# Kernel optimization log

Hardware: AMD Instinct MI355X
Metric: run time of the kernel (lower is better)

Reference implementation:

```python
import jax, jax.numpy as jnp
import numpy as np

B, P, C, H, W = 2, 4, 3, 256, 256
BGH, BGW = 2764, 3856
NOISE_MU, NOISE_SIGMA, NOISE_POISSON, BG_RATIO = 5.0, 1.0, 2.0, 0.1


def setup_inputs() -> dict:
    key = jax.random.key(0)
    k_x, k_bg = jax.random.split(key, 2)
    x = jax.random.uniform(k_x, (B, P, C, H, W), dtype=jnp.float32)
    t = jnp.array([0.05, 0.1, 0.15, 0.2], dtype=jnp.float32)          # Time_init (len p)
    ratio = jnp.ones((P,), dtype=jnp.float32)
    life = jnp.array([100.0, 200.0, 300.0], dtype=jnp.float32)         # flo_life (len c)
    intensity_ratio = jnp.array([1.0, 0.8, 0.6], dtype=jnp.float32)    # flo_intensity_ratio
    bg_file = jax.random.uniform(k_bg, (P, BGH, BGW), dtype=jnp.float32)
    return {"x": x, "t": t, "ratio": ratio, "life": life,
            "intensity_ratio": intensity_ratio, "bg_file": bg_file}


def reference(x, t, ratio, life, intensity_ratio, bg_file):
    b, p, c, h, w = x.shape
    key = jax.random.key(42)
    k_life, k_sig, k_norm, k_p1, k_p2, k_bg1, k_bg2, k_bgn, k_idx = jax.random.split(key, 9)

    # Time = relu((t*ratio)*1000), per-p scalar broadcast over (b,c,h,w)
    Time = jnp.maximum((t * ratio) * 1000.0, 0.0)                      # (p,)

    # tao_i: 9-point linspace around each lifetime, concatenated -> (T,) with T = 9*c
    tao = (life[:, None] + jnp.linspace(-40.0, 40.0, 9)).reshape(-1)   # (9c,)

    Life = life[None, None, :, None, None]                             # (1,1,c,1,1)
    Life_rand = Life + (jax.random.uniform(k_life, (b, p, c, h, w)) - 0.5) * 2.0 * 6.0
    sigma = 6.0
    sigma_rand = sigma + (jax.random.uniform(k_sig, (b, p, c, h, w)) - 0.5) * 2.0 * sigma * 0.05

    tao6 = tao[:, None, None, None, None, None]                        # (T,1,1,1,1,1)
    # Gaussian weights over the tao axis (matches torch's 3.14 constant)
    w_i = jnp.exp(-(tao6 - Life_rand) ** 2 / (2.0 * sigma_rand ** 2)) / (
        jnp.sqrt(jnp.float32(2.0 * 3.14)) * sigma_rand)                # (T,b,p,c,h,w)
    w_i = w_i / w_i.sum(axis=0)

    # tao_gt: sum over c, mean over p, permute -> (b,T,h,w), detached
    tao_gt = jax.lax.stop_gradient(jnp.transpose(w_i.sum(axis=3).mean(axis=2), (1, 0, 2, 3)))

    # decay_metrics = sum_T w_i * exp(-Time/tao); exp term only depends on (T,p)
    et = jnp.exp(-Time[None, :] / tao[:, None])                        # (T,p)
    decay = jnp.einsum('tp,tbpchw->bpchw', et, w_i)                    # (b,p,c,h,w)

    x2 = (x * decay * intensity_ratio[None, None, :, None, None]).sum(axis=2)  # (b,p,h,w)

    # noise(): Normal + Poisson(x/max) + Poisson(const) + x (samples detached in torch)
    xm = x2 / (x2.max() + 0.0001)
    n_int = xm * NOISE_MU + NOISE_SIGMA * jax.random.normal(k_norm, x2.shape)
    p_int = jax.random.poisson(k_p1, jnp.maximum(xm, 0.0)).astype(x2.dtype)
    pois = jax.random.poisson(k_p2, jnp.full(x2.shape, NOISE_POISSON)).astype(x2.dtype)
    x3 = n_int + p_int + pois + x2

    # bg(): scaled background file + noise, random 256x256 row offset
    bg1 = jax.random.uniform(k_bg1, (b, p, 1, 1)) * 0.5 + 0.5
    bg2 = jax.random.uniform(k_bg2, (b, p, 1, 1)) * 0.5 + 0.5
    bgn = jax.random.normal(k_bgn, (b, p, BGH, BGW))
    GRR = (bg_file[None] * bg1 + bgn * bg2) * BG_RATIO                 # (b,p,BGH,BGW)
    idx = jax.random.randint(k_idx, (), 0, 9)
    patch = jax.lax.dynamic_slice(GRR, (0, 0, idx, 0), (b, p, 256, 256))
    x4 = jnp.clip(x3 + patch, 0.0, 255.0) / 255.0

    return (x4, tao_gt, t * ratio, ratio)
```

## Files before the change

### kernel.cpp

```cpp
#include <hip/hip_runtime.h>
#include <cstdint>
#include <cstddef>

#define BB 2
#define PP 4
#define CC 3
#define HWSZ 65536
#define BGH 2764
#define BGW 3856
#define NTAO 27
#define X4_SIZE (BB*PP*HWSZ)
#define TAO_OFF X4_SIZE
#define TAO_SIZE (BB*NTAO*HWSZ)
#define OUT2_OFF (TAO_OFF + TAO_SIZE)
#define NPK 24
#define NBLK_A 2048

__host__ __device__ inline uint32_t rotl32(uint32_t x, int r) {
#ifdef __HIP_DEVICE_COMPILE__
  return __builtin_amdgcn_alignbit(x, x, 32 - r);
#else
  return (x << r) | (x >> (32 - r));
#endif
}

__host__ __device__ inline void tf2x32(uint32_t k0, uint32_t k1,
                                       uint32_t x0, uint32_t x1,
                                       uint32_t& o0, uint32_t& o1) {
  uint32_t ks2 = k0 ^ k1 ^ 0x1BD11BDAu;
  x0 += k0; x1 += k1;
#define TF_RND(r) { x0 += x1; x1 = rotl32(x1, r); x1 ^= x0; }
  TF_RND(13) TF_RND(15) TF_RND(26) TF_RND(6)
  x0 += k1;  x1 += ks2 + 1u;
  TF_RND(17) TF_RND(29) TF_RND(16) TF_RND(24)
  x0 += ks2; x1 += k0 + 2u;
  TF_RND(13) TF_RND(15) TF_RND(26) TF_RND(6)
  x0 += k0;  x1 += k1 + 3u;
  TF_RND(17) TF_RND(29) TF_RND(16) TF_RND(24)
  x0 += k1;  x1 += ks2 + 4u;
  TF_RND(13) TF_RND(15) TF_RND(26) TF_RND(6)
  x0 += ks2; x1 += k0 + 5u;
#undef TF_RND
  o0 = x0; o1 = x1;
}

__host__ __device__ inline uint32_t bits32(uint32_t k0, uint32_t k1, uint32_t e) {
  uint32_t o0, o1;
  tf2x32(k0, k1, 0u, e, o0, o1);
  return o0 ^ o1;
}

static void jax_split(uint32_t k0, uint32_t k1, int n, uint32_t (*keys)[2]) {
  for (int i = 0; i < n; ++i)
    tf2x32(k0, k1, 0u, (uint32_t)i, keys[i][0], keys[i][1]);
}

__host__ __device__ inline float u01(uint32_t bits) {
  uint32_t fb = (bits >> 9) | 0x3F800000u;
  return __builtin_bit_cast(float, fb) - 1.0f;
}

__device__ inline float erfinv_f(float x) {
  float w = -log1pf(-x * x);
  float p;
  if (w < 5.0f) {
    w = w - 2.5f;
    p = 2.81022636e-08f;
    p = fmaf(p, w, 3.43273939e-07f);
    p = fmaf(p, w, -3.5233877e-06f);
    p = fmaf(p, w, -4.39150654e-06f);
    p = fmaf(p, w, 0.00021858087f);
    p = fmaf(p, w, -0.00125372503f);
    p = fmaf(p, w, -0.00417768164f);
    p = fmaf(p, w, 0.246640727f);
    p = fmaf(p, w, 1.50140941f);
  } else {
    w = sqrtf(w) - 3.0f;
    p = -0.000200214257f;
    p = fmaf(p, w, 0.000100950558f);
    p = fmaf(p, w, 0.00134934322f);
    p = fmaf(p, w, -0.00367342844f);
    p = fmaf(p, w, 0.00573950773f);
    p = fmaf(p, w, -0.0076224613f);
    p = fmaf(p, w, 0.00943887047f);
    p = fmaf(p, w, 1.00167406f);
    p = fmaf(p, w, 2.83297682f);
  }
  return p * x;
}

__device__ inline float normal_e(uint32_t k0, uint32_t k1, uint32_t e) {
  float f = u01(bits32(k0, k1, e));
  const float LO = -0.99999994f;
  float u = fmaxf(LO, fmaf(f, 2.0f, LO));
  return 1.41421356237f * erfinv_f(u);
}

struct PCParams {
  uint32_t kn0, kn1;
  uint32_t kb0, kb1;
  uint32_t s1[NPK * 2];
  uint32_t s2[NPK * 2];
  float bg1[8], bg2[8];
  int idx;
};

__device__ inline float decay_pc(uint32_t kl0, uint32_t kl1, uint32_t ks0,
                                 uint32_t ks1, uint32_t e,
                                 const float (*et)[4], int p, float* tg9) {
  float ul = u01(bits32(kl0, kl1, e));
  float us = u01(bits32(ks0, ks1, e));
  float d0 = -40.0f - (ul - 0.5f) * 12.0f;
  float sr = fmaf(us - 0.5f, 0.6f, 6.0f);
  float inv = __builtin_amdgcn_rcpf(2.0f * sr * sr);
  float q[9];
  float A  = __expf(-20.0f * inv * d0);
  float Bm = __expf(-100.0f * inv);
  float B2 = Bm * Bm;
  q[0] = __expf(-(d0 * d0) * inv);
  float m = A * Bm;
  float s = q[0];
#pragma unroll
  for (int j = 1; j < 9; ++j) {
    q[j] = q[j - 1] * m;
    m *= B2;
    s += q[j];
  }
  float rs = __builtin_amdgcn_rcpf(s);
  float dec = 0.0f;
#pragma unroll
  for (int j = 0; j < 9; ++j) {
    float wn = q[j] * rs;
    tg9[j] += wn;
    dec = fmaf(et[j][p], wn, dec);
  }
  return dec;
}

__global__ __launch_bounds__(256) void kA(
    const float* __restrict__ x, const float* __restrict__ t,
    const float* __restrict__ ratio, const float* __restrict__ life,
    const float* __restrict__ inten, float* __restrict__ out,
    float* __restrict__ bmax,
    uint32_t kl0, uint32_t kl1, uint32_t ks0, uint32_t ks1) {
  __shared__ float tao_s[NTAO];
  __shared__ float et_s[NTAO][4];
  __shared__ float inten_s[3];
  __shared__ float tg_lds[4][9][64];
  __shared__ float bmax_s[4];
  const int tid = threadIdx.x;
  if (tid < NTAO * 4) {
    int j = tid >> 2, p = tid & 3;
    float tao = life[j / 9] + (-40.0f + 10.0f * (float)(j % 9));
    float Tp = fmaxf(t[p] * ratio[p] * 1000.0f, 0.0f);
    et_s[j][p] = expf((-Tp) / tao);
    if (p == 0) tao_s[j] = tao;
  }
  if (tid < 3) inten_s[tid] = inten[tid];
  __syncthreads();

  const int blk = blockIdx.x;
  const int b = blk >> 10;
  const int hwg = blk & 1023;
  const int p = tid >> 6;
  const int lane = tid & 63;
  const int hw = hwg * 64 + lane;

  float acc = 0.0f;

  for (int c = 0; c < 3; ++c) {
    float tg9[9];
#pragma unroll
    for (int j = 0; j < 9; ++j) tg9[j] = 0.0f;

    const uint32_t e = (uint32_t)((((b * 4 + p) * 3 + c) << 16) + hw);
    float dec = decay_pc(kl0, kl1, ks0, ks1, e,
                         (const float(*)[4])&et_s[c * 9], p, tg9);
    acc = fmaf(x[e] * dec, inten_s[c], acc);

#pragma unroll
    for (int j = 0; j < 9; ++j) tg_lds[p][j][lane] = tg9[j];
    __syncthreads();
    for (int jj = p; jj < 9; jj += 4) {
      float s = ((tg_lds[0][jj][lane] + tg_lds[1][jj][lane]) +
                 (tg_lds[2][jj][lane] + tg_lds[3][jj][lane]));
      out[TAO_OFF + ((b * NTAO + c * 9 + jj) << 16) + hw] = s * 0.25f;
    }
    __syncthreads();
  }

  out[((b * 4 + p) << 16) + hw] = acc;

  float m = acc;
#pragma unroll
  for (int off = 32; off; off >>= 1) m = fmaxf(m, __shfl_xor(m, off));
  if (lane == 0) bmax_s[p] = m;
  __syncthreads();
  if (tid == 0)
    bmax[blk] = fmaxf(fmaxf(bmax_s[0], bmax_s[1]),
                      fmaxf(bmax_s[2], bmax_s[3]));
}

__global__ __launch_bounds__(1024) void kMax(const float* __restrict__ bmax,
                                             float* __restrict__ maxslot) {
  __shared__ float red[16];
  const int tid = threadIdx.x;
  float m = fmaxf(bmax[tid], bmax[tid + 1024]);
#pragma unroll
  for (int off = 32; off; off >>= 1) m = fmaxf(m, __shfl_xor(m, off));
  if ((tid & 63) == 0) red[tid >> 6] = m;
  __syncthreads();
  if (tid == 0) {
    float mm = red[0];
#pragma unroll
    for (int i = 1; i < 16; ++i) mm = fmaxf(mm, red[i]);
    maxslot[0] = mm;
  }
}

__global__ __launch_bounds__(256) void kC(
    const float* __restrict__ bgf, const float* __restrict__ t,
    const float* __restrict__ ratio, float* __restrict__ out,
    const float* __restrict__ maxslot, PCParams pc) {
  const int e = blockIdx.x * 256 + threadIdx.x;
  if (blockIdx.x == 0 && threadIdx.x < 8) {
    int i = threadIdx.x;
    out[OUT2_OFF + i] = (i < 4) ? t[i] * ratio[i] : ratio[i - 4];
  }
  const int bp = e >> 16;
  const int rcc = e & 0xFFFF;
  const int r = rcc >> 8;
  const int cc = rcc & 255;

  const int row = pc.idx + r;
  const int p = bp & 3;
  float bg = bgf[(p * BGH + row) * BGW + cc];
  const uint32_t ebg = (uint32_t)((bp * BGH + row) * BGW + cc);
  float nb = normal_e(pc.kb0, pc.kb1, ebg);
  float patch = (bg * pc.bg1[bp] + nb * pc.bg2[bp]) * 0.1f;

  float n = normal_e(pc.kn0, pc.kn1, (uint32_t)e);

  const float x2 = out[e];
  const float mx = maxslot[0];
  const float xm = x2 / (mx + 0.0001f);
  float n_int = xm * 5.0f + 1.0f * n;

  float lam1 = fmaxf(xm, 0.0f);
  const bool z1 = !(lam1 > 0.0f);
  float lp1 = 0.0f, lp2 = 0.0f;
  int k1 = 0, k2 = 0;
#pragma clang loop unroll(disable)
  for (int i = 0; i < NPK; ++i) {
    bool c1 = (!z1) && (lp1 > -lam1);
    bool c2 = (lp2 > -2.0f);
    if (!(c1 || c2)) break;
    if (c1) { k1++; lp1 += __logf(u01(bits32(pc.s1[2*i], pc.s1[2*i+1], (uint32_t)e))); }
    if (c2) { k2++; lp2 += __logf(u01(bits32(pc.s2[2*i], pc.s2[2*i+1], (uint32_t)e))); }
  }
  float pi = z1 ? 0.0f : (float)(k1 - 1);
  float po = (float)(k2 - 1);

  float x3 = ((n_int + pi) + po) + x2;
  float v = x3 + patch;
  v = fminf(fmaxf(v, 0.0f), 255.0f);
  out[e] = v / 255.0f;
}

extern "C" void kernel_launch(void* const* d_in, const int* in_sizes, int n_in,
                              void* d_out, int out_size, void* d_ws, size_t ws_size,
                              hipStream_t stream) {
  const float* x     = (const float*)d_in[0];
  const float* t     = (const float*)d_in[1];
  const float* ratio = (const float*)d_in[2];
  const float* life  = (const float*)d_in[3];
  const float* inten = (const float*)d_in[4];
  const float* bgf   = (const float*)d_in[5];
  float* out = (float*)d_out;
  float* bmax = (float*)d_ws;
  float* maxslot = bmax + NBLK_A;

  uint32_t sk[9][2];
  jax_split(0u, 42u, 9, sk);

  PCParams pc;
  pc.kn0 = sk[2][0]; pc.kn1 = sk[2][1];
  pc.kb0 = sk[7][0]; pc.kb1 = sk[7][1];

  {
    uint32_t r0 = sk[3][0], r1 = sk[3][1];
    for (int i = 0; i < NPK; ++i) {
      uint32_t two[2][2];
      jax_split(r0, r1, 2, two);
      pc.s1[2*i] = two[1][0]; pc.s1[2*i+1] = two[1][1];
      r0 = two[0][0]; r1 = two[0][1];
    }
    r0 = sk[4][0]; r1 = sk[4][1];
    for (int i = 0; i < NPK; ++i) {
      uint32_t two[2][2];
      jax_split(r0, r1, 2, two);
      pc.s2[2*i] = two[1][0]; pc.s2[2*i+1] = two[1][1];
      r0 = two[0][0]; r1 = two[0][1];
    }
  }

  for (uint32_t i = 0; i < 8; ++i) {
    pc.bg1[i] = u01(bits32(sk[5][0], sk[5][1], i)) * 0.5f + 0.5f;
    pc.bg2[i] = u01(bits32(sk[6][0], sk[6][1], i)) * 0.5f + 0.5f;
  }

  {
    uint32_t hi = bits32(sk[8][0], sk[8][1], 0u);
    uint32_t lo = bits32(sk[8][0], sk[8][1], 1u);
    const uint32_t span = 9u;
    uint32_t mult = (65536u % span);
    mult = (mult * mult) % span;
    uint32_t off = ((hi % span) * mult + (lo % span)) % span;
    pc.idx = (int)off;
  }

  kA<<<NBLK_A, 256, 0, stream>>>(x, t, ratio, life, inten, out, bmax,
                                 sk[0][0], sk[0][1], sk[1][0], sk[1][1]);
  kMax<<<1, 1024, 0, stream>>>(bmax, maxslot);
  kC<<<X4_SIZE / 256, 256, 0, stream>>>(bgf, t, ratio, out, maxslot, pc);
}
```

Baseline: 40.52 us.

## Fold max reduction into kC, split noise work across thread pairs, batch tao_gt stores

Removes the separate single-block max kernel: every kC block now re-reduces the 2048 per-block maxima itself. kC launches two threads per output element, one doing the normal noise plus the const-rate Poisson loop and the other doing the background noise plus the data-dependent Poisson loop. Partial results are exchanged with a lane shuffle, so the serial Poisson loops of the two draws run in parallel rather than back to back. In kA, the tao_gt staging buffer now holds all three channels so only one barrier is needed, and the unused tao_s array is removed. The cost is redundant max reads in every kC block, twice as many kC threads, and more LDS per kA block.

```diff
diff --git a/kernel.cpp b/kernel.cpp
--- a/kernel.cpp
+++ b/kernel.cpp
@@ -143,10 +143,9 @@
     const float* __restrict__ inten, float* __restrict__ out,
     float* __restrict__ bmax,
     uint32_t kl0, uint32_t kl1, uint32_t ks0, uint32_t ks1) {
-  __shared__ float tao_s[NTAO];
   __shared__ float et_s[NTAO][4];
   __shared__ float inten_s[3];
-  __shared__ float tg_lds[4][9][64];
+  __shared__ float tg_lds[4][NTAO][64];
   __shared__ float bmax_s[4];
   const int tid = threadIdx.x;
   if (tid < NTAO * 4) {
@@ -154,7 +153,6 @@
     float tao = life[j / 9] + (-40.0f + 10.0f * (float)(j % 9));
     float Tp = fmaxf(t[p] * ratio[p] * 1000.0f, 0.0f);
     et_s[j][p] = expf((-Tp) / tao);
-    if (p == 0) tao_s[j] = tao;
   }
   if (tid < 3) inten_s[tid] = inten[tid];
   __syncthreads();
@@ -168,6 +166,7 @@
 
   float acc = 0.0f;
 
+#pragma unroll
   for (int c = 0; c < 3; ++c) {
     float tg9[9];
 #pragma unroll
@@ -179,14 +178,16 @@
     acc = fmaf(x[e] * dec, inten_s[c], acc);
 
 #pragma unroll
-    for (int j = 0; j < 9; ++j) tg_lds[p][j][lane] = tg9[j];
-    __syncthreads();
-    for (int jj = p; jj < 9; jj += 4) {
-      float s = ((tg_lds[0][jj][lane] + tg_lds[1][jj][lane]) +
-                 (tg_lds[2][jj][lane] + tg_lds[3][jj][lane]));
-      out[TAO_OFF + ((b * NTAO + c * 9 + jj) << 16) + hw] = s * 0.25f;
-    }
-    __syncthreads();
+    for (int j = 0; j < 9; ++j) tg_lds[p][c * 9 + j][lane] = tg9[j];
+  }
+  __syncthreads();
+
+#pragma unroll
+  for (int it = tid; it < NTAO * 64; it += 256) {
+    int row = it >> 6, ln = it & 63;
+    float s = ((tg_lds[0][row][ln] + tg_lds[1][row][ln]) +
+               (tg_lds[2][row][ln] + tg_lds[3][row][ln]));
+    out[TAO_OFF + ((b * NTAO + row) << 16) + hwg * 64 + ln] = s * 0.25f;
   }
 
   out[((b * 4 + p) << 16) + hw] = acc;
@@ -201,70 +202,82 @@
                       fmaxf(bmax_s[2], bmax_s[3]));
 }
 
-__global__ __launch_bounds__(1024) void kMax(const float* __restrict__ bmax,
-                                             float* __restrict__ maxslot) {
-  __shared__ float red[16];
-  const int tid = threadIdx.x;
-  float m = fmaxf(bmax[tid], bmax[tid + 1024]);
-#pragma unroll
-  for (int off = 32; off; off >>= 1) m = fmaxf(m, __shfl_xor(m, off));
-  if ((tid & 63) == 0) red[tid >> 6] = m;
-  __syncthreads();
-  if (tid == 0) {
-    float mm = red[0];
-#pragma unroll
-    for (int i = 1; i < 16; ++i) mm = fmaxf(mm, red[i]);
-    maxslot[0] = mm;
-  }
-}
-
 __global__ __launch_bounds__(256) void kC(
     const float* __restrict__ bgf, const float* __restrict__ t,
     const float* __restrict__ ratio, float* __restrict__ out,
-    const float* __restrict__ maxslot, PCParams pc) {
-  const int e = blockIdx.x * 256 + threadIdx.x;
-  if (blockIdx.x == 0 && threadIdx.x < 8) {
-    int i = threadIdx.x;
-    out[OUT2_OFF + i] = (i < 4) ? t[i] * ratio[i] : ratio[i - 4];
-  }
+    const float* __restrict__ bmax, PCParams pc) {
+  __shared__ float red_s[4];
+  __shared__ float mx_s;
+  const int tid = threadIdx.x;
+
+  float m = 0.0f;
+#pragma unroll
+  for (int k = 0; k < 8; ++k) m = fmaxf(m, bmax[tid + 256 * k]);
+#pragma unroll
+  for (int off = 32; off; off >>= 1) m = fmaxf(m, __shfl_xor(m, off));
+  if ((tid & 63) == 0) red_s[tid >> 6] = m;
+  __syncthreads();
+  if (tid == 0)
+    mx_s = fmaxf(fmaxf(red_s[0], red_s[1]), fmaxf(red_s[2], red_s[3]));
+  __syncthreads();
+  const float mx = mx_s;
+
+  if (blockIdx.x == 0 && tid < 8)
+    out[OUT2_OFF + tid] = (tid < 4) ? t[tid] * ratio[tid] : ratio[tid - 4];
+
+  const int t2 = blockIdx.x * 256 + tid;
+  const int e = t2 >> 1;
+  const int parity = t2 & 1;
+
   const int bp = e >> 16;
   const int rcc = e & 0xFFFF;
   const int r = rcc >> 8;
   const int cc = rcc & 255;
 
+  const float x2 = out[e];
+  const float xm = x2 * __builtin_amdgcn_rcpf(mx + 0.0001f);
+
   const int row = pc.idx + r;
-  const int p = bp & 3;
-  float bg = bgf[(p * BGH + row) * BGW + cc];
+  const int pp = bp & 3;
   const uint32_t ebg = (uint32_t)((bp * BGH + row) * BGW + cc);
-  float nb = normal_e(pc.kb0, pc.kb1, ebg);
-  float patch = (bg * pc.bg1[bp] + nb * pc.bg2[bp]) * 0.1f;
-
-  float n = normal_e(pc.kn0, pc.kn1, (uint32_t)e);
-
-  const float x2 = out[e];
-  const float mx = maxslot[0];
-  const float xm = x2 / (mx + 0.0001f);
-  float n_int = xm * 5.0f + 1.0f * n;
-
-  float lam1 = fmaxf(xm, 0.0f);
-  const bool z1 = !(lam1 > 0.0f);
-  float lp1 = 0.0f, lp2 = 0.0f;
-  int k1 = 0, k2 = 0;
+  uint32_t nk0 = parity ? pc.kb0 : pc.kn0;
+  uint32_t nk1 = parity ? pc.kb1 : pc.kn1;
+  uint32_t ne  = parity ? ebg : (uint32_t)e;
+  float nval = normal_e(nk0, nk1, ne);
+
+  float patch = 0.0f;
+  if (parity) {
+    float bg = bgf[(pp * BGH + row) * BGW + cc];
+    patch = (bg * pc.bg1[bp] + nval * pc.bg2[bp]) * 0.1f;
+  }
+
+  float lam = parity ? fmaxf(xm, 0.0f) : 2.0f;
+  const bool zz = !(lam > 0.0f);
+  const float neg = -lam;
+  float lp = 0.0f;
+  int k = 0;
 #pragma clang loop unroll(disable)
   for (int i = 0; i < NPK; ++i) {
-    bool c1 = (!z1) && (lp1 > -lam1);
-    bool c2 = (lp2 > -2.0f);
-    if (!(c1 || c2)) break;
-    if (c1) { k1++; lp1 += __logf(u01(bits32(pc.s1[2*i], pc.s1[2*i+1], (uint32_t)e))); }
-    if (c2) { k2++; lp2 += __logf(u01(bits32(pc.s2[2*i], pc.s2[2*i+1], (uint32_t)e))); }
-  }
-  float pi = z1 ? 0.0f : (float)(k1 - 1);
-  float po = (float)(k2 - 1);
-
-  float x3 = ((n_int + pi) + po) + x2;
-  float v = x3 + patch;
-  v = fminf(fmaxf(v, 0.0f), 255.0f);
-  out[e] = v / 255.0f;
+    bool c = (!zz) && (lp > neg);
+    if (!__any(c)) break;
+    if (c) {
+      k++;
+      uint32_t key0 = parity ? pc.s1[2 * i]     : pc.s2[2 * i];
+      uint32_t key1 = parity ? pc.s1[2 * i + 1] : pc.s2[2 * i + 1];
+      lp += __logf(u01(bits32(key0, key1, (uint32_t)e)));
+    }
+  }
+  float pk = zz ? 0.0f : (float)(k - 1);
+
+  float pi_o    = __shfl_xor(pk, 1);
+  float patch_o = __shfl_xor(patch, 1);
+
+  if (!parity) {
+    float n_int = fmaf(xm, 5.0f, nval);
+    float v = (((n_int + pi_o) + pk) + x2) + patch_o;
+    v = fminf(fmaxf(v, 0.0f), 255.0f);
+    out[e] = v * (1.0f / 255.0f);
+  }
 }
 
 extern "C" void kernel_launch(void* const* d_in, const int* in_sizes, int n_in,
@@ -278,7 +291,6 @@
   const float* bgf   = (const float*)d_in[5];
   float* out = (float*)d_out;
   float* bmax = (float*)d_ws;
-  float* maxslot = bmax + NBLK_A;
 
   uint32_t sk[9][2];
   jax_split(0u, 42u, 9, sk);
@@ -321,6 +333,5 @@
 
   kA<<<NBLK_A, 256, 0, stream>>>(x, t, ratio, life, inten, out, bmax,
                                  sk[0][0], sk[0][1], sk[1][0], sk[1][1]);
-  kMax<<<1, 1024, 0, stream>>>(bmax, maxslot);
-  kC<<<X4_SIZE / 256, 256, 0, stream>>>(bgf, t, ratio, out, maxslot, pc);
-}
+  kC<<<(2 * X4_SIZE) / 256, 256, 0, stream>>>(bgf, t, ratio, out, bmax, pc);
+}
```

After: 43.27 us. 6.8% more time.

## Fuse max reduction into kC, batch Poisson sampling, use fast intrinsics

Applied to the files above, without the earlier changes.

Removes the separate single-block max kernel: each kC block re-reduces the 2048 per-block maxima itself, saving one launch and its serialization gap at the cost of redundant reads. The Poisson sampling loop is rewritten to process four uniforms per step with wave-uniform (__any) exit checks, reducing branch divergence and loop overhead but computing some extra random numbers. erfinv, the normalization and the final scaling switch to fast log, sqrt, rcp and multiply intrinsics, which may change precision slightly.

```diff
diff --git a/kernel.cpp b/kernel.cpp
--- a/kernel.cpp
+++ b/kernel.cpp
@@ -14,6 +14,7 @@
 #define TAO_SIZE (BB*NTAO*HWSZ)
 #define OUT2_OFF (TAO_OFF + TAO_SIZE)
 #define NPK 24
+#define NPB 4
 #define NBLK_A 2048
 
 __host__ __device__ inline uint32_t rotl32(uint32_t x, int r) {
@@ -61,7 +62,7 @@
 }
 
 __device__ inline float erfinv_f(float x) {
-  float w = -log1pf(-x * x);
+  float w = -__logf(fmaf(-x, x, 1.0f));
   float p;
   if (w < 5.0f) {
     w = w - 2.5f;
@@ -75,7 +76,7 @@
     p = fmaf(p, w, 0.246640727f);
     p = fmaf(p, w, 1.50140941f);
   } else {
-    w = sqrtf(w) - 3.0f;
+    w = __builtin_amdgcn_sqrtf(w) - 3.0f;
     p = -0.000200214257f;
     p = fmaf(p, w, 0.000100950558f);
     p = fmaf(p, w, 0.00134934322f);
@@ -104,6 +105,23 @@
   float bg1[8], bg2[8];
   int idx;
 };
+
+__device__ inline void pk_batch(const uint32_t* __restrict__ sk, int b,
+                                uint32_t e, float neg, float& lp, int& k) {
+  float l0 = __logf(u01(bits32(sk[(b*NPB+0)*2], sk[(b*NPB+0)*2+1], e)));
+  float l1 = __logf(u01(bits32(sk[(b*NPB+1)*2], sk[(b*NPB+1)*2+1], e)));
+  float l2 = __logf(u01(bits32(sk[(b*NPB+2)*2], sk[(b*NPB+2)*2+1], e)));
+  float l3 = __logf(u01(bits32(sk[(b*NPB+3)*2], sk[(b*NPB+3)*2+1], e)));
+  int cnt = (lp > neg) ? 1 : 0;
+  float p0 = lp + l0;
+  cnt += (p0 > neg) ? 1 : 0;
+  float p1 = p0 + l1;
+  cnt += (p1 > neg) ? 1 : 0;
+  float p2 = p1 + l2;
+  cnt += (p2 > neg) ? 1 : 0;
+  lp = p2 + l3;
+  k += cnt;
+}
 
 __device__ inline float decay_pc(uint32_t kl0, uint32_t kl1, uint32_t ks0,
                                  uint32_t ks1, uint32_t e,
@@ -143,7 +161,6 @@
     const float* __restrict__ inten, float* __restrict__ out,
     float* __restrict__ bmax,
     uint32_t kl0, uint32_t kl1, uint32_t ks0, uint32_t ks1) {
-  __shared__ float tao_s[NTAO];
   __shared__ float et_s[NTAO][4];
   __shared__ float inten_s[3];
   __shared__ float tg_lds[4][9][64];
@@ -154,7 +171,6 @@
     float tao = life[j / 9] + (-40.0f + 10.0f * (float)(j % 9));
     float Tp = fmaxf(t[p] * ratio[p] * 1000.0f, 0.0f);
     et_s[j][p] = expf((-Tp) / tao);
-    if (p == 0) tao_s[j] = tao;
   }
   if (tid < 3) inten_s[tid] = inten[tid];
   __syncthreads();
@@ -201,32 +217,30 @@
                       fmaxf(bmax_s[2], bmax_s[3]));
 }
 
-__global__ __launch_bounds__(1024) void kMax(const float* __restrict__ bmax,
-                                             float* __restrict__ maxslot) {
-  __shared__ float red[16];
-  const int tid = threadIdx.x;
-  float m = fmaxf(bmax[tid], bmax[tid + 1024]);
-#pragma unroll
-  for (int off = 32; off; off >>= 1) m = fmaxf(m, __shfl_xor(m, off));
-  if ((tid & 63) == 0) red[tid >> 6] = m;
-  __syncthreads();
-  if (tid == 0) {
-    float mm = red[0];
-#pragma unroll
-    for (int i = 1; i < 16; ++i) mm = fmaxf(mm, red[i]);
-    maxslot[0] = mm;
-  }
-}
-
 __global__ __launch_bounds__(256) void kC(
     const float* __restrict__ bgf, const float* __restrict__ t,
     const float* __restrict__ ratio, float* __restrict__ out,
-    const float* __restrict__ maxslot, PCParams pc) {
-  const int e = blockIdx.x * 256 + threadIdx.x;
-  if (blockIdx.x == 0 && threadIdx.x < 8) {
-    int i = threadIdx.x;
-    out[OUT2_OFF + i] = (i < 4) ? t[i] * ratio[i] : ratio[i - 4];
-  }
+    const float* __restrict__ bmax, PCParams pc) {
+  __shared__ float red_s[4];
+  __shared__ float mx_s;
+  const int tid = threadIdx.x;
+
+  float m = 0.0f;
+#pragma unroll
+  for (int k = 0; k < 8; ++k) m = fmaxf(m, bmax[tid + 256 * k]);
+#pragma unroll
+  for (int off = 32; off; off >>= 1) m = fmaxf(m, __shfl_xor(m, off));
+  if ((tid & 63) == 0) red_s[tid >> 6] = m;
+  __syncthreads();
+  if (tid == 0)
+    mx_s = fmaxf(fmaxf(red_s[0], red_s[1]), fmaxf(red_s[2], red_s[3]));
+  __syncthreads();
+  const float mx = mx_s;
+
+  if (blockIdx.x == 0 && tid < 8)
+    out[OUT2_OFF + tid] = (tid < 4) ? t[tid] * ratio[tid] : ratio[tid - 4];
+
+  const int e = blockIdx.x * 256 + tid;
   const int bp = e >> 16;
   const int rcc = e & 0xFFFF;
   const int r = rcc >> 8;
@@ -234,29 +248,29 @@
 
   const int row = pc.idx + r;
   const int p = bp & 3;
-  float bg = bgf[(p * BGH + row) * BGW + cc];
+  const float bg = bgf[(p * BGH + row) * BGW + cc];
+  const float x2 = out[e];
+
   const uint32_t ebg = (uint32_t)((bp * BGH + row) * BGW + cc);
   float nb = normal_e(pc.kb0, pc.kb1, ebg);
+  float n  = normal_e(pc.kn0, pc.kn1, (uint32_t)e);
   float patch = (bg * pc.bg1[bp] + nb * pc.bg2[bp]) * 0.1f;
 
-  float n = normal_e(pc.kn0, pc.kn1, (uint32_t)e);
-
-  const float x2 = out[e];
-  const float mx = maxslot[0];
-  const float xm = x2 / (mx + 0.0001f);
-  float n_int = xm * 5.0f + 1.0f * n;
+  const float xm = x2 * __builtin_amdgcn_rcpf(mx + 0.0001f);
+  float n_int = fmaf(xm, 5.0f, n);
 
   float lam1 = fmaxf(xm, 0.0f);
   const bool z1 = !(lam1 > 0.0f);
+  const float neg1 = -lam1;
   float lp1 = 0.0f, lp2 = 0.0f;
   int k1 = 0, k2 = 0;
 #pragma clang loop unroll(disable)
-  for (int i = 0; i < NPK; ++i) {
-    bool c1 = (!z1) && (lp1 > -lam1);
-    bool c2 = (lp2 > -2.0f);
-    if (!(c1 || c2)) break;
-    if (c1) { k1++; lp1 += __logf(u01(bits32(pc.s1[2*i], pc.s1[2*i+1], (uint32_t)e))); }
-    if (c2) { k2++; lp2 += __logf(u01(bits32(pc.s2[2*i], pc.s2[2*i+1], (uint32_t)e))); }
+  for (int b = 0; b < NPK / NPB; ++b) {
+    bool a1 = __any((!z1) && (lp1 > neg1));
+    bool a2 = __any(lp2 > -2.0f);
+    if (!(a1 || a2)) break;
+    if (a1) pk_batch(pc.s1, b, (uint32_t)e, neg1, lp1, k1);
+    if (a2) pk_batch(pc.s2, b, (uint32_t)e, -2.0f, lp2, k2);
   }
   float pi = z1 ? 0.0f : (float)(k1 - 1);
   float po = (float)(k2 - 1);
@@ -264,7 +278,7 @@
   float x3 = ((n_int + pi) + po) + x2;
   float v = x3 + patch;
   v = fminf(fmaxf(v, 0.0f), 255.0f);
-  out[e] = v / 255.0f;
+  out[e] = v * (1.0f / 255.0f);
 }
 
 extern "C" void kernel_launch(void* const* d_in, const int* in_sizes, int n_in,
@@ -278,7 +292,6 @@
   const float* bgf   = (const float*)d_in[5];
   float* out = (float*)d_out;
   float* bmax = (float*)d_ws;
-  float* maxslot = bmax + NBLK_A;
 
   uint32_t sk[9][2];
   jax_split(0u, 42u, 9, sk);
@@ -321,6 +334,5 @@
 
   kA<<<NBLK_A, 256, 0, stream>>>(x, t, ratio, life, inten, out, bmax,
                                  sk[0][0], sk[0][1], sk[1][0], sk[1][1]);
-  kMax<<<1, 1024, 0, stream>>>(bmax, maxslot);
-  kC<<<X4_SIZE / 256, 256, 0, stream>>>(bgf, t, ratio, out, maxslot, pc);
-}
+  kC<<<X4_SIZE / 256, 256, 0, stream>>>(bgf, t, ratio, out, bmax, pc);
+}
```

After: 39.53 us. 1.03x faster.
